# Optimization experiments

Hardware: AMD Instinct MI355X
Metric: run time of the kernel (lower is better)

The kernel has to match this reference:

```python
import math
import jax, jax.numpy as jnp
import numpy as np

EMBED_DIM = 1024
NUM_HEADS = 16
HEAD_DIM = EMBED_DIM // NUM_HEADS
B, S = 4, 2048


def setup_inputs() -> dict:
    key = jax.random.key(0)
    ks = jax.random.split(key, 12)
    sc = 1.0 / math.sqrt(EMBED_DIM)
    inp = {
        "query": jax.random.normal(ks[0], (B, S, EMBED_DIM), jnp.float32),
        "key": jax.random.normal(ks[1], (B, S, EMBED_DIM), jnp.float32),
        "value": jax.random.normal(ks[2], (B, S, EMBED_DIM), jnp.float32),
        # causal mask: True = masked (upper triangle above diagonal)
        "attn_mask": jnp.triu(jnp.ones((S, S), jnp.bool_), k=1),
        "q_w": jax.random.normal(ks[3], (EMBED_DIM, EMBED_DIM), jnp.float32) * sc,
        "q_b": jax.random.normal(ks[4], (EMBED_DIM,), jnp.float32) * sc,
        "k_w": jax.random.normal(ks[5], (EMBED_DIM, EMBED_DIM), jnp.float32) * sc,
        "k_b": jax.random.normal(ks[6], (EMBED_DIM,), jnp.float32) * sc,
        "v_w": jax.random.normal(ks[7], (EMBED_DIM, EMBED_DIM), jnp.float32) * sc,
        "v_b": jax.random.normal(ks[8], (EMBED_DIM,), jnp.float32) * sc,
        "o_w": jax.random.normal(ks[9], (EMBED_DIM, EMBED_DIM), jnp.float32) * sc,
        "o_b": jax.random.normal(ks[10], (EMBED_DIM,), jnp.float32) * sc,
    }
    return inp


def _split_heads(x):
    # (B, S, E) -> (B, H, S, D)
    b, s, _ = x.shape
    return x.reshape(b, s, NUM_HEADS, HEAD_DIM).transpose(0, 2, 1, 3)


def reference(query, key, value, attn_mask, q_w, q_b, k_w, k_b, v_w, v_b, o_w, o_b):
    # torch Linear: y = x @ W.T + b
    q = _split_heads(query @ q_w.T + q_b)
    k = _split_heads(key @ k_w.T + k_b)
    v = _split_heads(value @ v_w.T + v_b)
    scale = math.sqrt(HEAD_DIM)
    scores = jnp.einsum("bhqd,bhkd->bhqk", q, k) / scale
    scores = jnp.where(attn_mask[None, None, :, :], -jnp.inf, scores)
    attn = jax.nn.softmax(scores, axis=-1)
    ctx = jnp.einsum("bhqk,bhkd->bhqd", attn, v)  # (B,H,S,D)
    ctx = ctx.transpose(0, 2, 1, 3).reshape(query.shape[0], query.shape[1], EMBED_DIM)
    return ctx @ o_w.T + o_b
```

## Files before the change

### kernel.cpp

```cpp
#include <hip/hip_runtime.h>
#include <stdint.h>

#define BB 4
#define SS 2048
#define EE 1024
#define HH 16
#define DD 64
#define MM (BB*SS)

typedef unsigned short u16;
typedef __attribute__((ext_vector_type(8))) short bf16x8;
typedef __attribute__((ext_vector_type(4))) float f32x4;

#define MFMA __builtin_amdgcn_mfma_f32_16x16x32_bf16

#if __has_builtin(__builtin_amdgcn_exp2f)
#define EXP2(x) __builtin_amdgcn_exp2f(x)
#else
#define EXP2(x) exp2f(x)
#endif

__device__ __forceinline__ u16 f2bf(float f) {
  union { float f; uint32_t u; } x; x.f = f;
  uint32_t r = (x.u + 0x7fffu + ((x.u >> 16) & 1u)) >> 16;
  return (u16)r;
}

__device__ __forceinline__ uint32_t cvtpk(float lo, float hi) {
  uint32_t r;
  asm volatile("v_cvt_pk_bf16_f32 %0, %1, %2" : "=v"(r) : "v"(lo), "v"(hi));
  return r;
}

__device__ __forceinline__ void gl_lds16(const void* g, void* l) {
  __builtin_amdgcn_global_load_lds(
      (const __attribute__((address_space(1))) uint32_t*)g,
      (__attribute__((address_space(3))) uint32_t*)l, 16, 0, 0);
}

__global__ __launch_bounds__(256) void cast_all(
    const float* __restrict__ a0, const float* __restrict__ a1,
    const float* __restrict__ a2,
    const float* __restrict__ w0, const float* __restrict__ w1,
    const float* __restrict__ w2, const float* __restrict__ w3,
    u16* __restrict__ da0, u16* __restrict__ da1, u16* __restrict__ da2,
    u16* __restrict__ dw0, u16* __restrict__ dw1,
    u16* __restrict__ dw2, u16* __restrict__ dw3) {
  int i = blockIdx.x * 256 + threadIdx.x;
  const float* s; u16* d; int off;
  if (i < 3 * (1 << 20)) {
    int sel = i >> 20; off = i & ((1 << 20) - 1);
    s = sel == 0 ? a0 : sel == 1 ? a1 : a2;
    d = sel == 0 ? da0 : sel == 1 ? da1 : da2;
  } else {
    int k = i - 3 * (1 << 20);
    int sel = k >> 17; off = k & ((1 << 17) - 1);
    s = sel == 0 ? w0 : sel == 1 ? w1 : sel == 2 ? w2 : w3;
    d = sel == 0 ? dw0 : sel == 1 ? dw1 : sel == 2 ? dw2 : dw3;
  }
  const float4* sp = (const float4*)s;
  float4 a = sp[off*2], b = sp[off*2+1];
  union { u16 h[8]; uint4 v; } o;
  o.h[0]=f2bf(a.x); o.h[1]=f2bf(a.y); o.h[2]=f2bf(a.z); o.h[3]=f2bf(a.w);
  o.h[4]=f2bf(b.x); o.h[5]=f2bf(b.y); o.h[6]=f2bf(b.z); o.h[7]=f2bf(b.w);
  *(uint4*)(d + (size_t)off*8) = o.v;
}

template<int OUT_BF16>
__device__ __forceinline__ void gemm_body(
    const u16* __restrict__ A, const u16* __restrict__ W,
    const float* __restrict__ bias, void* __restrict__ Cout,
    int Ndim, int Kdim, float scale, int m0, int n0,
    u16* As, u16* Bs) {
  const int tid = threadIdx.x;
  const int lane = tid & 63, w = tid >> 6;
  const int wr = w >> 1, wc = w & 1;
  const int srow = tid >> 2;
  const int scol = (tid & 3) * 8;

  f32x4 acc[4][4] = {};

  const u16* ag = A + (size_t)(m0 + srow) * Kdim + scol;
  const u16* bg = W + (size_t)(n0 + srow) * Kdim + scol;
  const size_t rstride = (size_t)64 * Kdim;
  const int l15 = lane & 15;
  const int fke = (lane >> 4) * 8;

  for (int k0 = 0; k0 < Kdim; k0 += 32) {
    gl_lds16(ag + k0,           As + tid*8);
    gl_lds16(ag + k0 + rstride, As + 2048 + tid*8);
    gl_lds16(bg + k0,           Bs + tid*8);
    gl_lds16(bg + k0 + rstride, Bs + 2048 + tid*8);
    __syncthreads();

    bf16x8 af[4], bfr[4];
    #pragma unroll
    for (int m = 0; m < 4; ++m)
      af[m] = *(const bf16x8*)(As + (wr*64 + m*16 + l15)*32 + fke);
    #pragma unroll
    for (int n = 0; n < 4; ++n)
      bfr[n] = *(const bf16x8*)(Bs + (wc*64 + n*16 + l15)*32 + fke);
    #pragma unroll
    for (int m = 0; m < 4; ++m)
      #pragma unroll
      for (int n = 0; n < 4; ++n)
        acc[m][n] = MFMA(af[m], bfr[n], acc[m][n], 0, 0, 0);
    __syncthreads();
  }

  const int ccol = wc*64 + l15;
  float bv[4];
  #pragma unroll
  for (int n = 0; n < 4; ++n) bv[n] = bias[n0 + ccol + n*16];
  #pragma unroll
  for (int m = 0; m < 4; ++m) {
    #pragma unroll
    for (int i = 0; i < 4; ++i) {
      size_t row = (size_t)(m0 + wr*64 + m*16 + (lane>>4)*4 + i);
      #pragma unroll
      for (int n = 0; n < 4; ++n) {
        float v = (acc[m][n][i] + bv[n]) * scale;
        size_t idx = row * Ndim + (n0 + ccol + n*16);
        if (OUT_BF16) ((u16*)Cout)[idx] = f2bf(v);
        else          ((float*)Cout)[idx] = v;
      }
    }
  }
}

__global__ __launch_bounds__(256, 2) void gemm_qkv(
    const u16* __restrict__ qx, const u16* __restrict__ kx, const u16* __restrict__ vx,
    const u16* __restrict__ wqm, const u16* __restrict__ wkm, const u16* __restrict__ wvm,
    const float* __restrict__ qbv, const float* __restrict__ kbv, const float* __restrict__ vbv,
    u16* __restrict__ qo, u16* __restrict__ ko, u16* __restrict__ vo) {
  __shared__ alignas(16) u16 As[128*32];
  __shared__ alignas(16) u16 Bs[128*32];
  const int flat = blockIdx.x + blockIdx.y * 8 + blockIdx.z * 512;
  const int j = flat & 7, s = flat >> 3;
  const int c = 3*j + (s >> 6), i = s & 63;
  const int nx = i & 7, yy = ((c & 7) << 3) + (i >> 3);
  const int z = c >> 3;
  const u16* A = z == 0 ? qx : z == 1 ? kx : vx;
  const u16* W = z == 0 ? wqm : z == 1 ? wkm : wvm;
  const float* bias = z == 0 ? qbv : z == 1 ? kbv : vbv;
  u16* C = z == 0 ? qo : z == 1 ? ko : vo;
  const float scale = z == 0 ? 0.125f : 1.0f;
  gemm_body<1>(A, W, bias, C, EE, EE, scale, yy * 128, nx * 128, As, Bs);
}

__global__ __launch_bounds__(256, 2) void gemm_out(
    const u16* __restrict__ A, const u16* __restrict__ W,
    const float* __restrict__ bias, float* __restrict__ Cout) {
  __shared__ alignas(16) u16 As[128*32];
  __shared__ alignas(16) u16 Bs[128*32];
  const int flat = blockIdx.x + blockIdx.y * 8;
  const int j = flat & 7, s = flat >> 3;
  const int nx = s & 7, yy = (j << 3) + (s >> 3);
  gemm_body<0>(A, W, bias, Cout, EE, EE, 1.0f, yy * 128, nx * 128, As, Bs);
}

__global__ __launch_bounds__(256, 2) void attn9(
    const u16* __restrict__ Q, const u16* __restrict__ K,
    const u16* __restrict__ V, u16* __restrict__ ctx) {
  __shared__ alignas(16) u16 Ks[2][2][64*64];
  __shared__ alignas(16) u16 VTs[2][2][64*64];
  __shared__ alignas(16) u16 Ps[4][32*64];

  const int tid = threadIdx.x, lane = tid & 63, w = tid >> 6;
  const int l15 = lane & 15, l4 = lane >> 4;

  const int f = blockIdx.x;
  const int j = f & 7, s = f >> 3;
  const int qlo = s & 7;
  const int panel = j * 8 + (s >> 3);
  const int h = panel & 15, b = panel >> 4;
  const size_t base = ((size_t)b * SS) * EE + h * DD;

  const int kr  = tid >> 3;
  const int ksl = tid & 7;
  const int rv  = tid >> 2;
  const int vc  = tid & 3;

  u16* KsE  = (u16*)Ks;
  u16* VTsE = (u16*)VTs;
  u16* PsE  = (u16*)Ps + w * 2048;

  auto stageK = [&](int t, int pb, int sub) {
    #pragma unroll
    for (int i = 0; i < 2; ++i) {
      int row = i*32 + kr;
      gl_lds16(K + base + (size_t)(t*64 + row)*EE + (ksl ^ (row & 7))*8,
               KsE + pb*8192 + sub*4096 + i*2048 + tid*8);
    }
  };
  auto vtWrite = [&](int pb, int sub, bf16x8 v0, bf16x8 v1) {
    #pragma unroll
    for (int jj = 0; jj < 16; ++jj) {
      u16 val = jj < 8 ? (u16)v0[jj] : (u16)v1[jj - 8];
      int d = vc*16 + jj;
      int sl = (rv >> 3) ^ (jj & 7) ^ (vc << 1);
      VTsE[pb*8192 + sub*4096 + d*64 + sl*8 + (rv & 7)] = val;
    }
  };

  #pragma unroll 1
  for (int pass = 0; pass < 2; ++pass) {
    const int qblk = pass == 0 ? (15 - qlo) : qlo;
    const int q0 = qblk * 128, wq = q0 + w * 32;
    const int npairs = qblk + 1;

    bf16x8 qf[2][2];
    #pragma unroll
    for (int G = 0; G < 2; ++G)
      #pragma unroll
      for (int kc = 0; kc < 2; ++kc)
        qf[G][kc] = *(const bf16x8*)(Q + base + (size_t)(wq + G*16 + l15)*EE + kc*32 + l4*8);

    f32x4 o[2][4] = {};
    float lsum[2] = {0.f, 0.f};

    auto computeTile = [&](int t, int pb, int sub) {
      if (wq + 31 < t*64) return;
      const bool g0act = (wq + 15 >= t*64);
      const u16* tileK = KsE + pb*8192 + sub*4096;
      const u16* tileV = VTsE + pb*8192 + sub*4096;

      f32x4 sc[2][4] = {};
      #pragma unroll
      for (int nt = 0; nt < 4; ++nt) {
        int row = nt*16 + l15;
        int sw = row & 7;
        const u16* kb = tileK + row*64;
        bf16x8 kf0 = *(const bf16x8*)(kb + ((l4    ) ^ sw)*8);
        bf16x8 kf1 = *(const bf16x8*)(kb + ((4 + l4) ^ sw)*8);
        sc[1][nt] = MFMA(kf0, qf[1][0], sc[1][nt], 0, 0, 0);
        sc[1][nt] = MFMA(kf1, qf[1][1], sc[1][nt], 0, 0, 0);
        if (g0act) {
          sc[0][nt] = MFMA(kf0, qf[0][0], sc[0][nt], 0, 0, 0);
          sc[0][nt] = MFMA(kf1, qf[0][1], sc[0][nt], 0, 0, 0);
        }
      }

      #pragma unroll
      for (int G = 0; G < 2; ++G) {
        if (G == 0 && !g0act) continue;
        const bool nomask = (t*64 + 63 <= wq + G*16);
        const int qg = wq + G*16 + l15;
        #pragma unroll
        for (int nt = 0; nt < 4; ++nt) {
          float p0 = EXP2(__builtin_fmaf(sc[G][nt][0], 1.44269504f, -17.3123405f));
          float p1 = EXP2(__builtin_fmaf(sc[G][nt][1], 1.44269504f, -17.3123405f));
          float p2 = EXP2(__builtin_fmaf(sc[G][nt][2], 1.44269504f, -17.3123405f));
          float p3 = EXP2(__builtin_fmaf(sc[G][nt][3], 1.44269504f, -17.3123405f));
          if (!nomask) {
            int kvs = t*64 + nt*16 + l4*4;
            if (kvs + 0 > qg) p0 = 0.f;
            if (kvs + 1 > qg) p1 = 0.f;
            if (kvs + 2 > qg) p2 = 0.f;
            if (kvs + 3 > qg) p3 = 0.f;
          }
          lsum[G] += (p0 + p1) + (p2 + p3);
          uint2 pk;
          pk.x = cvtpk(p0, p1);
          pk.y = cvtpk(p2, p3);
          *(uint2*)((char*)PsE + (G*16 + l15)*128
                        + (((nt*2 + (l4 >> 1)) ^ (l15 & 7)) * 16)
                        + (l4 & 1) * 8) = pk;
        }
      }

      #pragma unroll
      for (int cc = 0; cc < 2; ++cc) {
        bf16x8 pf1 = *(const bf16x8*)((char*)PsE + (16 + l15)*128
                                     + (((cc*4 + l4) ^ (l15 & 7)) * 16));
        bf16x8 pf0;
        if (g0act)
          pf0 = *(const bf16x8*)((char*)PsE + l15*128
                                     + (((cc*4 + l4) ^ (l15 & 7)) * 16));
        #pragma unroll
        for (int dm = 0; dm < 4; ++dm) {
          int sl = (cc*4 + l4) ^ (l15 & 7) ^ (dm << 1);
          bf16x8 vfv = *(const bf16x8*)(tileV + (dm*16 + l15)*64 + sl*8);
          o[1][dm] = MFMA(pf1, vfv, o[1][dm], 0, 0, 0);
          if (g0act) o[0][dm] = MFMA(pf0, vfv, o[0][dm], 0, 0, 0);
        }
      }
    };

    {
      const u16* va = V + base + (size_t)rv*EE + vc*16;
      const u16* vb = V + base + (size_t)(64 + rv)*EE + vc*16;
      bf16x8 a0 = *(const bf16x8*)va, a1 = *(const bf16x8*)(va + 8);
      bf16x8 b0 = *(const bf16x8*)vb, b1 = *(const bf16x8*)(vb + 8);
      stageK(0, 0, 0);
      stageK(1, 0, 1);
      vtWrite(0, 0, a0, a1);
      vtWrite(0, 1, b0, b1);
    }
    __syncthreads();

    for (int u = 0; u < npairs; ++u) {
      const int cur = u & 1;
      const bool havenext = (u + 1 < npairs);
      bf16x8 na0, na1, nb0, nb1;
      if (havenext) {
        const u16* va = V + base + (size_t)((2*u+2)*64 + rv)*EE + vc*16;
        const u16* vb = V + base + (size_t)((2*u+3)*64 + rv)*EE + vc*16;
        na0 = *(const bf16x8*)va; na1 = *(const bf16x8*)(va + 8);
        nb0 = *(const bf16x8*)vb; nb1 = *(const bf16x8*)(vb + 8);
        stageK(2*u+2, cur ^ 1, 0);
        stageK(2*u+3, cur ^ 1, 1);
      }

      computeTile(2*u, cur, 0);
      if (havenext) vtWrite(cur ^ 1, 0, na0, na1);
      computeTile(2*u + 1, cur, 1);
      if (havenext) vtWrite(cur ^ 1, 1, nb0, nb1);
      __syncthreads();
    }

    #pragma unroll
    for (int G = 0; G < 2; ++G) {
      float r = lsum[G];
      r += __shfl_xor(r, 16);
      r += __shfl_xor(r, 32);
      lsum[G] = 1.0f / r;
    }

    #pragma unroll
    for (int G = 0; G < 2; ++G)
      #pragma unroll
      for (int i = 0; i < 4; ++i) {
        float invv = __shfl(lsum[G], l4*4 + i);
        size_t roff = base + (size_t)(wq + G*16 + l4*4 + i) * EE;
        #pragma unroll
        for (int dm = 0; dm < 4; ++dm)
          ctx[roff + dm*16 + l15] = f2bf(o[G][dm][i] * invv);
      }
  }
}

extern "C" void kernel_launch(void* const* d_in, const int* in_sizes, int n_in,
                              void* d_out, int out_size, void* d_ws, size_t ws_size,
                              hipStream_t stream) {
  const float* query = (const float*)d_in[0];
  const float* key   = (const float*)d_in[1];
  const float* value = (const float*)d_in[2];
  const float* q_w = (const float*)d_in[4];
  const float* q_b = (const float*)d_in[5];
  const float* k_w = (const float*)d_in[6];
  const float* k_b = (const float*)d_in[7];
  const float* v_w = (const float*)d_in[8];
  const float* v_b = (const float*)d_in[9];
  const float* o_w = (const float*)d_in[10];
  const float* o_b = (const float*)d_in[11];

  char* ws = (char*)d_ws;
  const size_t XB = (size_t)MM * EE * 2;
  const size_t WB = (size_t)EE * EE * 2;
  u16* qx = (u16*)(ws);
  u16* kx = (u16*)(ws + XB);
  u16* vx = (u16*)(ws + 2*XB);
  u16* wq = (u16*)(ws + 3*XB);
  u16* wk = (u16*)(ws + 3*XB + WB);
  u16* wv = (u16*)(ws + 3*XB + 2*WB);
  u16* wo = (u16*)(ws + 3*XB + 3*WB);
  u16* qp = (u16*)(ws + 3*XB + 4*WB);
  u16* kp = (u16*)(ws + 4*XB + 4*WB);
  u16* vp = (u16*)(ws + 5*XB + 4*WB);
  u16* ctxb = qx;

  const int ncast = 3 * (1 << 20) + 4 * (1 << 17);
  cast_all<<<ncast/256, 256, 0, stream>>>(query, key, value,
                                          q_w, k_w, v_w, o_w,
                                          qx, kx, vx, wq, wk, wv, wo);

  gemm_qkv<<<dim3(EE/128, MM/128, 3), 256, 0, stream>>>(
      qx, kx, vx, wq, wk, wv, q_b, k_b, v_b, qp, kp, vp);

  attn9<<<512, 256, 0, stream>>>(qp, kp, vp, ctxb);

  gemm_out<<<dim3(EE/128, MM/128), 256, 0, stream>>>(ctxb, wo, o_b, (float*)d_out);
}
```

Before: 183.9 us.

## Fuse fp32-to-bf16 activation cast into QKV GEMM A-tile load

The QKV projection GEMM now loads fp32 activations directly into LDS with an XOR swizzle and converts them to bf16 in registers before the MFMA, so the cast kernel only handles the weights. This removes a full write and read of three bf16 activation buffers (about 48MB of traffic) and shrinks the cast launch. The block-to-tile mapping is also reworked for the new grid ordering. In exchange the A tile doubles in LDS size, global-to-LDS traffic for A doubles per k-step, and conversion instructions sit in the inner loop.

```diff
diff --git a/kernel.cpp b/kernel.cpp
--- a/kernel.cpp
+++ b/kernel.cpp
@@ -38,26 +38,15 @@
       (__attribute__((address_space(3))) uint32_t*)l, 16, 0, 0);
 }
 
-__global__ __launch_bounds__(256) void cast_all(
-    const float* __restrict__ a0, const float* __restrict__ a1,
-    const float* __restrict__ a2,
-    const float* __restrict__ w0, const float* __restrict__ w1,
-    const float* __restrict__ w2, const float* __restrict__ w3,
-    u16* __restrict__ da0, u16* __restrict__ da1, u16* __restrict__ da2,
-    u16* __restrict__ dw0, u16* __restrict__ dw1,
-    u16* __restrict__ dw2, u16* __restrict__ dw3) {
+__global__ __launch_bounds__(256) void cast_w(
+    const float* __restrict__ s0, const float* __restrict__ s1,
+    const float* __restrict__ s2, const float* __restrict__ s3,
+    u16* __restrict__ d0, u16* __restrict__ d1,
+    u16* __restrict__ d2, u16* __restrict__ d3) {
   int i = blockIdx.x * 256 + threadIdx.x;
-  const float* s; u16* d; int off;
-  if (i < 3 * (1 << 20)) {
-    int sel = i >> 20; off = i & ((1 << 20) - 1);
-    s = sel == 0 ? a0 : sel == 1 ? a1 : a2;
-    d = sel == 0 ? da0 : sel == 1 ? da1 : da2;
-  } else {
-    int k = i - 3 * (1 << 20);
-    int sel = k >> 17; off = k & ((1 << 17) - 1);
-    s = sel == 0 ? w0 : sel == 1 ? w1 : sel == 2 ? w2 : w3;
-    d = sel == 0 ? dw0 : sel == 1 ? dw1 : sel == 2 ? dw2 : dw3;
-  }
+  int sel = i >> 17, off = i & ((1 << 17) - 1);
+  const float* s = sel == 0 ? s0 : sel == 1 ? s1 : sel == 2 ? s2 : s3;
+  u16* d = sel == 0 ? d0 : sel == 1 ? d1 : sel == 2 ? d2 : d3;
   const float4* sp = (const float4*)s;
   float4 a = sp[off*2], b = sp[off*2+1];
   union { u16 h[8]; uint4 v; } o;
@@ -66,37 +55,67 @@
   *(uint4*)(d + (size_t)off*8) = o.v;
 }
 
-template<int OUT_BF16>
+template<int A_FP32, int OUT_BF16>
 __device__ __forceinline__ void gemm_body(
-    const u16* __restrict__ A, const u16* __restrict__ W,
+    const void* __restrict__ Ap, const u16* __restrict__ W,
     const float* __restrict__ bias, void* __restrict__ Cout,
     int Ndim, int Kdim, float scale, int m0, int n0,
     u16* As, u16* Bs) {
   const int tid = threadIdx.x;
   const int lane = tid & 63, w = tid >> 6;
   const int wr = w >> 1, wc = w & 1;
+  const int l15 = lane & 15;
+  const int l4 = lane >> 4;
+  const int fke = l4 * 8;
+
+  f32x4 acc[4][4] = {};
+
   const int srow = tid >> 2;
   const int scol = (tid & 3) * 8;
-
-  f32x4 acc[4][4] = {};
-
-  const u16* ag = A + (size_t)(m0 + srow) * Kdim + scol;
   const u16* bg = W + (size_t)(n0 + srow) * Kdim + scol;
-  const size_t rstride = (size_t)64 * Kdim;
-  const int l15 = lane & 15;
-  const int fke = (lane >> 4) * 8;
+  const size_t rstrideB = (size_t)64 * Kdim;
+
+  const int ar  = tid >> 3;
+  const int asl = tid & 7;
+  const int asw = asl ^ (ar & 7);
+  const float* agf = nullptr;
+  const u16*   agh = nullptr;
+  if (A_FP32) agf = (const float*)Ap + (size_t)(m0 + ar) * Kdim + asw * 4;
+  else        agh = (const u16*)Ap + (size_t)(m0 + srow) * Kdim + scol;
+
+  char* AsB = (char*)As;
 
   for (int k0 = 0; k0 < Kdim; k0 += 32) {
-    gl_lds16(ag + k0,           As + tid*8);
-    gl_lds16(ag + k0 + rstride, As + 2048 + tid*8);
-    gl_lds16(bg + k0,           Bs + tid*8);
-    gl_lds16(bg + k0 + rstride, Bs + 2048 + tid*8);
+    if (A_FP32) {
+      #pragma unroll
+      for (int i = 0; i < 4; ++i)
+        gl_lds16(agf + (size_t)i*32*Kdim + k0, AsB + i*4096 + tid*16);
+    } else {
+      gl_lds16(agh + k0,                     As + tid*8);
+      gl_lds16(agh + k0 + (size_t)64*Kdim,   As + 2048 + tid*8);
+    }
+    gl_lds16(bg + k0,            Bs + tid*8);
+    gl_lds16(bg + k0 + rstrideB, Bs + 2048 + tid*8);
     __syncthreads();
 
     bf16x8 af[4], bfr[4];
     #pragma unroll
-    for (int m = 0; m < 4; ++m)
-      af[m] = *(const bf16x8*)(As + (wr*64 + m*16 + l15)*32 + fke);
+    for (int m = 0; m < 4; ++m) {
+      int r = wr*64 + m*16 + l15;
+      if (A_FP32) {
+        const char* rb = AsB + r*128;
+        f32x4 fa = *(const f32x4*)(rb + (((l4*2    ) ^ (r & 7)) * 16));
+        f32x4 fb = *(const f32x4*)(rb + (((l4*2 + 1) ^ (r & 7)) * 16));
+        union { uint32_t u[4]; bf16x8 v; } cv;
+        cv.u[0] = cvtpk(fa[0], fa[1]);
+        cv.u[1] = cvtpk(fa[2], fa[3]);
+        cv.u[2] = cvtpk(fb[0], fb[1]);
+        cv.u[3] = cvtpk(fb[2], fb[3]);
+        af[m] = cv.v;
+      } else {
+        af[m] = *(const bf16x8*)(As + r*32 + fke);
+      }
+    }
     #pragma unroll
     for (int n = 0; n < 4; ++n)
       bfr[n] = *(const bf16x8*)(Bs + (wc*64 + n*16 + l15)*32 + fke);
@@ -116,7 +135,7 @@
   for (int m = 0; m < 4; ++m) {
     #pragma unroll
     for (int i = 0; i < 4; ++i) {
-      size_t row = (size_t)(m0 + wr*64 + m*16 + (lane>>4)*4 + i);
+      size_t row = (size_t)(m0 + wr*64 + m*16 + l4*4 + i);
       #pragma unroll
       for (int n = 0; n < 4; ++n) {
         float v = (acc[m][n][i] + bv[n]) * scale;
@@ -129,23 +148,24 @@
 }
 
 __global__ __launch_bounds__(256, 2) void gemm_qkv(
-    const u16* __restrict__ qx, const u16* __restrict__ kx, const u16* __restrict__ vx,
+    const float* __restrict__ qx, const float* __restrict__ kx, const float* __restrict__ vx,
     const u16* __restrict__ wqm, const u16* __restrict__ wkm, const u16* __restrict__ wvm,
     const float* __restrict__ qbv, const float* __restrict__ kbv, const float* __restrict__ vbv,
     u16* __restrict__ qo, u16* __restrict__ ko, u16* __restrict__ vo) {
-  __shared__ alignas(16) u16 As[128*32];
+  __shared__ alignas(16) u16 As[128*64];
   __shared__ alignas(16) u16 Bs[128*32];
   const int flat = blockIdx.x + blockIdx.y * 8 + blockIdx.z * 512;
   const int j = flat & 7, s = flat >> 3;
-  const int c = 3*j + (s >> 6), i = s & 63;
-  const int nx = i & 7, yy = ((c & 7) << 3) + (i >> 3);
-  const int z = c >> 3;
-  const u16* A = z == 0 ? qx : z == 1 ? kx : vx;
+  const int c = 6*j + (s >> 5), i = s & 31;
+  const int nx = i & 7;
+  const int my = ((c & 15) << 2) + (i >> 3);
+  const int z = c >> 4;
+  const float* A = z == 0 ? qx : z == 1 ? kx : vx;
   const u16* W = z == 0 ? wqm : z == 1 ? wkm : wvm;
   const float* bias = z == 0 ? qbv : z == 1 ? kbv : vbv;
   u16* C = z == 0 ? qo : z == 1 ? ko : vo;
   const float scale = z == 0 ? 0.125f : 1.0f;
-  gemm_body<1>(A, W, bias, C, EE, EE, scale, yy * 128, nx * 128, As, Bs);
+  gemm_body<1,1>(A, W, bias, C, EE, EE, scale, my * 128, nx * 128, As, Bs);
 }
 
 __global__ __launch_bounds__(256, 2) void gemm_out(
@@ -156,7 +176,7 @@
   const int flat = blockIdx.x + blockIdx.y * 8;
   const int j = flat & 7, s = flat >> 3;
   const int nx = s & 7, yy = (j << 3) + (s >> 3);
-  gemm_body<0>(A, W, bias, Cout, EE, EE, 1.0f, yy * 128, nx * 128, As, Bs);
+  gemm_body<0,0>(A, W, bias, Cout, EE, EE, 1.0f, yy * 128, nx * 128, As, Bs);
 }
 
 __global__ __launch_bounds__(256, 2) void attn9(
@@ -358,25 +378,20 @@
   char* ws = (char*)d_ws;
   const size_t XB = (size_t)MM * EE * 2;
   const size_t WB = (size_t)EE * EE * 2;
-  u16* qx = (u16*)(ws);
-  u16* kx = (u16*)(ws + XB);
-  u16* vx = (u16*)(ws + 2*XB);
-  u16* wq = (u16*)(ws + 3*XB);
-  u16* wk = (u16*)(ws + 3*XB + WB);
-  u16* wv = (u16*)(ws + 3*XB + 2*WB);
-  u16* wo = (u16*)(ws + 3*XB + 3*WB);
-  u16* qp = (u16*)(ws + 3*XB + 4*WB);
-  u16* kp = (u16*)(ws + 4*XB + 4*WB);
-  u16* vp = (u16*)(ws + 5*XB + 4*WB);
-  u16* ctxb = qx;
-
-  const int ncast = 3 * (1 << 20) + 4 * (1 << 17);
-  cast_all<<<ncast/256, 256, 0, stream>>>(query, key, value,
-                                          q_w, k_w, v_w, o_w,
-                                          qx, kx, vx, wq, wk, wv, wo);
-
-  gemm_qkv<<<dim3(EE/128, MM/128, 3), 256, 0, stream>>>(
-      qx, kx, vx, wq, wk, wv, q_b, k_b, v_b, qp, kp, vp);
+  u16* wq = (u16*)(ws);
+  u16* wk = (u16*)(ws + WB);
+  u16* wv = (u16*)(ws + 2*WB);
+  u16* wo = (u16*)(ws + 3*WB);
+  u16* qp = (u16*)(ws + 4*WB);
+  u16* kp = (u16*)(ws + 4*WB + XB);
+  u16* vp = (u16*)(ws + 4*WB + 2*XB);
+  u16* ctxb = (u16*)(ws + 4*WB + 3*XB);
+
+  const int nw8 = EE * EE / 8;
+  cast_w<<<4*nw8/256, 256, 0, stream>>>(q_w, k_w, v_w, o_w, wq, wk, wv, wo);
+
+  gemm_qkv<<<dim3(8, 64, 3), 256, 0, stream>>>(
+      query, key, value, wq, wk, wv, q_b, k_b, v_b, qp, kp, vp);
 
   attn9<<<512, 256, 0, stream>>>(qp, kp, vp, ctxb);
 
```

Result: faster. 175.6 us (-4.5%).
